# Performance work log

Hardware: AMD Instinct MI355X
Metric: run time of the kernel (lower is better)

## Reference

```python
import jax, jax.numpy as jnp
import numpy as np

BETA = 0.95      # leak
THRESH = 1.0     # snntorch Leaky default threshold
ALPHA = 2.0      # ATan surrogate alpha (atan_with_alpha)
T = 100          # SPIKE_STEPS
D_IN = 65536     # input_dims
HID = 256        # fc1 hidden (hardcoded)
N_OUT = 20       # n_actions(2) * NUM_NEURONS_PER_ACTION(10)


def spike_fn(x):
    # forward of snntorch surrogate.ATan: Heaviside
    return (x > 0.0).astype(x.dtype)


def lif_step(mem, cur):
    # snntorch Leaky, reset_mechanism='subtract':
    # reset computed from previous membrane (detached), then decay+integrate, then fire
    reset = jax.lax.stop_gradient((mem > THRESH).astype(mem.dtype))
    mem_new = BETA * mem + cur - reset * THRESH
    spk = spike_fn(mem_new - THRESH)
    return spk, mem_new


def _run_net(x, W1, b1, W2, b2):
    # x: [T, D_IN]. Precompute all layer-1 currents as one big GEMM, then scan the recurrence.
    cur1_all = x @ W1.T + b1  # [T, HID]

    def step(carry, cur1):
        mem1, mem2 = carry
        spk1, mem1 = lif_step(mem1, cur1)
        cur2 = spk1 @ W2.T + b2  # [n_out]
        spk2, mem2 = lif_step(mem2, cur2)
        return (mem1, mem2), spk2

    init = (jnp.zeros((W1.shape[0],), x.dtype), jnp.zeros((W2.shape[0],), x.dtype))
    (_, mem2_final), spk2_hist = jax.lax.scan(step, init, cur1_all)
    return spk2_hist, mem2_final  # [T, n_out], [n_out]


def setup_inputs() -> dict:
    key = jax.random.key(0)
    ks = jax.random.split(key, 5)
    s = 0.01
    return {
        "poisson_spikes": jax.random.uniform(ks[0], (T, 1, D_IN), dtype=jnp.float32),
        "aW1": jax.random.normal(ks[1], (HID, D_IN), dtype=jnp.float32) * s,
        "ab1": jnp.zeros((HID,), jnp.float32),
        "aW2": jax.random.normal(ks[2], (N_OUT, HID), dtype=jnp.float32) * s,
        "ab2": jnp.zeros((N_OUT,), jnp.float32),
        "cW1": jax.random.normal(ks[3], (HID, D_IN), dtype=jnp.float32) * s,
        "cb1": jnp.zeros((HID,), jnp.float32),
        "cW2": jax.random.normal(ks[4], (1, HID), dtype=jnp.float32) * s,
        "cb2": jnp.zeros((1,), jnp.float32),
    }


def reference(poisson_spikes, aW1, ab1, aW2, ab2, cW1, cb1, cW2, cb2):
    x = poisson_spikes[:, 0, :]  # effective batch of 1 -> [T, D_IN]
    actor_spk_hist, _ = _run_net(x, aW1, ab1, aW2, ab2)        # [T, 20]
    _, critic_mem = _run_net(x, cW1, cb1, cW2, cb2)            # [1]
    spk_sum = actor_spk_hist.sum(axis=0)                       # [20] (sum over timesteps)
    action_vals = jnp.stack([spk_sum[:10].sum(), spk_sum[10:].sum()])
    policy = jax.nn.softmax(action_vals)                       # [2]
    return policy, critic_mem
```

## Files before the change

kernel.cpp:

```cpp
#include <hip/hip_runtime.h>
#include <hip/hip_bf16.h>

#define T_STEPS 100
#define D_IN    65536
#define HID     256
#define HTOT    512
#define BETA    0.95f
#define THRESH  1.0f

typedef __bf16 bf16x8 __attribute__((ext_vector_type(8)));
typedef float  f32x16 __attribute__((ext_vector_type(16)));

__device__ __forceinline__ void gload_lds16(const void* g, void* l) {
    __builtin_amdgcn_global_load_lds(
        (const __attribute__((address_space(1))) void*)g,
        (__attribute__((address_space(3))) void*)l, 16, 0, 0);
}

__global__ __launch_bounds__(512) void k_xpack(
    const float* __restrict__ x, __bf16* __restrict__ xp)
{
    const int idx  = blockIdx.x * 512 + threadIdx.x;
    const int slot = idx & 3;
    const int r    = (idx >> 2) & 127;
    const int gk   = idx >> 9;

    float f[8] = {0.f, 0.f, 0.f, 0.f, 0.f, 0.f, 0.f, 0.f};
    if (r < T_STEPS) {
        const float* src = x + (size_t)r * D_IN + gk * 32 + slot * 8;
        float4 v0 = *(const float4*)src;
        float4 v1 = *(const float4*)(src + 4);
        f[0] = v0.x; f[1] = v0.y; f[2] = v0.z; f[3] = v0.w;
        f[4] = v1.x; f[5] = v1.y; f[6] = v1.z; f[7] = v1.w;
    }
    bf16x8 hi, mi;
#pragma unroll
    for (int e = 0; e < 8; e++) {
        __bf16 h = (__bf16)f[e];
        hi[e] = h; mi[e] = (__bf16)(f[e] - (float)h);
    }
    const int G = r * 4 + (slot ^ ((r >> 1) & 3));
    __bf16* blob = xp + (size_t)gk * 8192;
    *(bf16x8*)(blob + G * 8)        = hi;
    *(bf16x8*)(blob + 4096 + G * 8) = mi;
}

__global__ __launch_bounds__(512, 4) void k_gemm1(
    const float* __restrict__ aW1,
    const float* __restrict__ cW1,
    const __bf16* __restrict__ xp,
    float* __restrict__ P,
    int nsteps)
{
    const int ht   = blockIdx.x;
    const int s    = blockIdx.y;
    const int tid  = threadIdx.x;
    const int lane = tid & 63;
    const int l31  = lane & 31;
    const int wv   = tid >> 6;
    const int wt   = (wv & 1) * 64;
    const int hq   = (wv >> 1) * 32;

    __shared__ __align__(16) char smem[2][32768];

    const float* Wbase = (ht < 2) ? (aW1 + (size_t)ht * 128 * D_IN)
                                  : (cW1 + (size_t)(ht - 2) * 128 * D_IN);

    const int gx0 = wv * 64 + lane;
    const int gx1 = 512 + gx0;
    const int wr0 = gx0 >> 3, wj0 = gx0 & 7;
    const int wr1 = gx1 >> 3, wj1 = gx1 & 7;
    const float* wsrc0 = Wbase + (size_t)wr0 * D_IN + (wj0 ^ (wr0 & 7)) * 4;
    const float* wsrc1 = Wbase + (size_t)wr1 * D_IN + (wj1 ^ (wr1 & 7)) * 4;
    const int gk0 = s * nsteps;

    f32x16 acc0, acc1;
#pragma unroll
    for (int i = 0; i < 16; i++) { acc0[i] = 0.f; acc1[i] = 0.f; }

#define STAGE(i) do {                                                         \
    char* b_ = smem[(i) & 1];                                                 \
    const __bf16* xb_ = xp + (size_t)(gk0 + (i)) * 8192;                      \
    const int kc_ = (gk0 + (i)) * 32;                                         \
    gload_lds16(xb_ + gx0 * 8, b_ + gx0 * 16);                                \
    gload_lds16(xb_ + gx1 * 8, b_ + gx1 * 16);                                \
    gload_lds16(wsrc0 + kc_, b_ + 16384 + gx0 * 16);                          \
    gload_lds16(wsrc1 + kc_, b_ + 16384 + gx1 * 16);                          \
} while (0)

#define COMPUTE(i) do {                                                       \
    const char* b_ = smem[(i) & 1];                                           \
    _Pragma("unroll")                                                         \
    for (int s16 = 0; s16 < 2; s16++) {                                       \
        const int hr = hq + l31;                                              \
        const int gb = s16 * 4 + (lane >> 5) * 2;                             \
        const char* wrow_ = b_ + 16384 + hr * 128;                            \
        float4 wa = *(const float4*)(wrow_ + ((gb ^ (hr & 7)) * 16));         \
        float4 wb = *(const float4*)(wrow_ + (((gb + 1) ^ (hr & 7)) * 16));   \
        float fb[8] = {wa.x, wa.y, wa.z, wa.w, wb.x, wb.y, wb.z, wb.w};       \
        bf16x8 bh, bm;                                                        \
        _Pragma("unroll")                                                     \
        for (int e = 0; e < 8; e++) {                                         \
            __bf16 h = (__bf16)fb[e];                                         \
            bh[e] = h; bm[e] = (__bf16)(fb[e] - (float)h);                    \
        }                                                                     \
        const int slot = s16 * 2 + (lane >> 5);                               \
        const int r0 = wt + l31, r1 = r0 + 32;                                \
        const int G0 = r0 * 4 + (slot ^ ((r0 >> 1) & 3));                     \
        const int G1 = r1 * 4 + (slot ^ ((r1 >> 1) & 3));                     \
        bf16x8 a0h = *(const bf16x8*)(b_ + G0 * 16);                          \
        bf16x8 a0m = *(const bf16x8*)(b_ + 8192 + G0 * 16);                   \
        bf16x8 a1h = *(const bf16x8*)(b_ + G1 * 16);                          \
        bf16x8 a1m = *(const bf16x8*)(b_ + 8192 + G1 * 16);                   \
        acc0 = __builtin_amdgcn_mfma_f32_32x32x16_bf16(a0m, bh, acc0, 0,0,0); \
        acc0 = __builtin_amdgcn_mfma_f32_32x32x16_bf16(a0h, bm, acc0, 0,0,0); \
        acc0 = __builtin_amdgcn_mfma_f32_32x32x16_bf16(a0h, bh, acc0, 0,0,0); \
        acc1 = __builtin_amdgcn_mfma_f32_32x32x16_bf16(a1m, bh, acc1, 0,0,0); \
        acc1 = __builtin_amdgcn_mfma_f32_32x32x16_bf16(a1h, bm, acc1, 0,0,0); \
        acc1 = __builtin_amdgcn_mfma_f32_32x32x16_bf16(a1h, bh, acc1, 0,0,0); \
    }                                                                         \
} while (0)

    STAGE(0);
    STAGE(1);
    for (int i = 0; i < nsteps; i++) {
        if (i + 1 < nsteps) asm volatile("s_waitcnt vmcnt(4)" ::: "memory");
        else                asm volatile("s_waitcnt vmcnt(0)" ::: "memory");
        __builtin_amdgcn_s_barrier();
        __builtin_amdgcn_sched_barrier(0);
        COMPUTE(i);
        __builtin_amdgcn_s_barrier();
        __builtin_amdgcn_sched_barrier(0);
        if (i + 2 < nsteps) STAGE(i + 2);
    }
#undef STAGE
#undef COMPUTE

    const int rbase = 4 * (lane >> 5);
    const int hcol  = ht * 128 + hq + l31;
    float* Pb = P + (size_t)s * T_STEPS * HTOT;
#pragma unroll
    for (int reg = 0; reg < 16; reg++) {
        const int row = (reg & 3) + rbase + 8 * (reg >> 2);
        const int t0  = wt + row;
        const int t1  = wt + 32 + row;
        if (t0 < T_STEPS) Pb[(size_t)t0 * HTOT + hcol] = acc0[reg];
        if (t1 < T_STEPS) Pb[(size_t)t1 * HTOT + hcol] = acc1[reg];
    }
}

__global__ __launch_bounds__(256) void k_reduce(
    const float* __restrict__ P,
    const float* __restrict__ ab1, const float* __restrict__ cb1,
    float* __restrict__ cur1, int NS)
{
    int g4 = blockIdx.x * 256 + threadIdx.x;
    int g  = g4 * 4;
    int h0 = g & (HTOT - 1);
    float4 sum;
    sum.x = (h0 + 0 < HID) ? ab1[h0 + 0] : cb1[h0 + 0 - HID];
    sum.y = (h0 + 1 < HID) ? ab1[h0 + 1] : cb1[h0 + 1 - HID];
    sum.z = (h0 + 2 < HID) ? ab1[h0 + 2] : cb1[h0 + 2 - HID];
    sum.w = (h0 + 3 < HID) ? ab1[h0 + 3] : cb1[h0 + 3 - HID];
    for (int ss = 0; ss < NS; ss++) {
        float4 v = *(const float4*)(P + (size_t)ss * T_STEPS * HTOT + g);
        sum.x += v.x; sum.y += v.y; sum.z += v.z; sum.w += v.w;
    }
    *(float4*)(cur1 + g) = sum;
}

__global__ __launch_bounds__(64) void k_lif1(
    const float* __restrict__ cur1,
    unsigned long long* __restrict__ bitsws,
    float* __restrict__ wsa)
{
    const int b    = blockIdx.x;
    const int lane = threadIdx.x;
    const int n    = b * 64 + lane;

    float mem = 0.f;
    for (int tb = 0; tb < T_STEPS; tb += 10) {
        float c[10];
#pragma unroll
        for (int i = 0; i < 10; i++) c[i] = cur1[(size_t)(tb + i) * HTOT + n];
#pragma unroll
        for (int i = 0; i < 10; i++) {
            float reset = (mem > THRESH) ? THRESH : 0.f;
            mem = BETA * mem + c[i] - reset;
            unsigned long long m = __ballot(mem > THRESH);
            if (lane == 0) bitsws[(size_t)(tb + i) * 8 + b] = m;
        }
    }
    if (b == 0 && lane == 0) { wsa[0] = 0.f; wsa[1] = 0.f; }
}

__global__ __launch_bounds__(128) void k_gemm2(
    const unsigned long long* __restrict__ bitsws,
    const float* __restrict__ aW2, const float* __restrict__ ab2,
    const float* __restrict__ cW2, const float* __restrict__ cb2,
    float* __restrict__ wsa, float* __restrict__ out)
{
    const int j   = blockIdx.x;
    const int tid = threadIdx.x;

    __shared__ float W[256];
    __shared__ float c2[T_STEPS];

    const float* Wsrc = (j < 20) ? (aW2 + j * 256) : cW2;
    for (int i = tid; i < 256; i += 128) W[i] = Wsrc[i];
    const float bias  = (j < 20) ? ab2[j] : cb2[0];
    const int   wbase = (j < 20) ? 0 : 4;
    __syncthreads();

    const int t = tid;
    if (t < T_STEPS) {
        unsigned long long m0 = bitsws[(size_t)t * 8 + wbase + 0];
        unsigned long long m1 = bitsws[(size_t)t * 8 + wbase + 1];
        unsigned long long m2 = bitsws[(size_t)t * 8 + wbase + 2];
        unsigned long long m3 = bitsws[(size_t)t * 8 + wbase + 3];
        float acc = bias;
#pragma unroll
        for (int bitp = 0; bitp < 64; bitp++) {
            acc += ((m0 >> bitp) & 1ULL) ? W[bitp]       : 0.f;
            acc += ((m1 >> bitp) & 1ULL) ? W[64 + bitp]  : 0.f;
            acc += ((m2 >> bitp) & 1ULL) ? W[128 + bitp] : 0.f;
            acc += ((m3 >> bitp) & 1ULL) ? W[192 + bitp] : 0.f;
        }
        c2[t] = acc;
    }
    __syncthreads();

    if (tid == 0) {
        float mem = 0.f, spk = 0.f;
        for (int tt = 0; tt < T_STEPS; tt++) {
            float reset = (mem > THRESH) ? THRESH : 0.f;
            mem = BETA * mem + c2[tt] - reset;
            spk += (mem > THRESH) ? 1.f : 0.f;
        }
        if (j < 10)       atomicAdd(&wsa[0], spk);
        else if (j < 20)  atomicAdd(&wsa[1], spk);
        else              out[2] = mem;
    }
}

__global__ __launch_bounds__(64) void k_final(
    const float* __restrict__ wsa, float* __restrict__ out)
{
    if (threadIdx.x == 0) {
        float a0 = wsa[0], a1 = wsa[1];
        float mx = fmaxf(a0, a1);
        float e0 = expf(a0 - mx), e1 = expf(a1 - mx);
        float inv = 1.f / (e0 + e1);
        out[0] = e0 * inv;
        out[1] = e1 * inv;
    }
}

extern "C" void kernel_launch(void* const* d_in, const int* in_sizes, int n_in,
                              void* d_out, int out_size, void* d_ws, size_t ws_size,
                              hipStream_t stream) {
    const float* x   = (const float*)d_in[0];
    const float* aW1 = (const float*)d_in[1];
    const float* ab1 = (const float*)d_in[2];
    const float* aW2 = (const float*)d_in[3];
    const float* ab2 = (const float*)d_in[4];
    const float* cW1 = (const float*)d_in[5];
    const float* cb1 = (const float*)d_in[6];
    const float* cW2 = (const float*)d_in[7];
    const float* cb2 = (const float*)d_in[8];
    float* out = (float*)d_out;

    const size_t xpack_bytes = 2048ull * 16384;
    int NS = 128;
    while (NS > 8 &&
           xpack_bytes + ((size_t)(NS + 1) * T_STEPS * HTOT) * sizeof(float)
               + 8192 > ws_size)
        NS >>= 1;
    const int nsteps = (D_IN / NS) / 32;

    __bf16* xpack = (__bf16*)d_ws;
    float*  P     = (float*)((char*)d_ws + xpack_bytes);
    float*  cur1  = P + (size_t)NS * T_STEPS * HTOT;
    unsigned long long* bitsws =
        (unsigned long long*)(cur1 + T_STEPS * HTOT);
    float* wsa = (float*)(bitsws + T_STEPS * 8);

    k_xpack <<<2048, 512, 0, stream>>>(x, xpack);
    k_gemm1 <<<dim3(4, NS), 512, 0, stream>>>(aW1, cW1, xpack, P, nsteps);
    k_reduce<<<(T_STEPS * HTOT / 4) / 256, 256, 0, stream>>>(P, ab1, cb1, cur1, NS);
    k_lif1  <<<8, 64, 0, stream>>>(cur1, bitsws, wsa);
    k_gemm2 <<<21, 128, 0, stream>>>(bitsws, aW2, ab2, cW2, cb2, wsa, out);
    k_final <<<1, 64, 0, stream>>>(wsa, out);
}
```

Baseline: 107.7 us.

## Stream x fragments from global in gemm1 and stage only W in LDS

k_gemm1 now uses 256-thread blocks, each covering 64 hidden units, on an 8xNS grid. Only the fp32 W tile goes into double-buffered LDS, now 64 K-columns deep. The packed bf16 hi/lo x fragments are loaded straight from global/L2 inside the compute loop instead of being staged through LDS. k_xpack is remapped so each thread reads contiguous columns of one x row, and it drops its slot swizzle to match the new direct reads. This frees LDS and raises occupancy, at the cost of more global/L2 traffic for x (read by 8 hidden tiles instead of 4) and x-load latency exposed inside the MFMA loop.

```diff
diff --git a/kernel.cpp b/kernel.cpp
--- a/kernel.cpp
+++ b/kernel.cpp
@@ -21,13 +21,13 @@
     const float* __restrict__ x, __bf16* __restrict__ xp)
 {
     const int idx  = blockIdx.x * 512 + threadIdx.x;
-    const int slot = idx & 3;
-    const int r    = (idx >> 2) & 127;
-    const int gk   = idx >> 9;
+    const int r    = idx >> 13;
+    const int cidx = idx & 8191;
+    const int col  = cidx * 8;
 
     float f[8] = {0.f, 0.f, 0.f, 0.f, 0.f, 0.f, 0.f, 0.f};
     if (r < T_STEPS) {
-        const float* src = x + (size_t)r * D_IN + gk * 32 + slot * 8;
+        const float* src = x + (size_t)r * D_IN + col;
         float4 v0 = *(const float4*)src;
         float4 v1 = *(const float4*)(src + 4);
         f[0] = v0.x; f[1] = v0.y; f[2] = v0.z; f[3] = v0.w;
@@ -39,13 +39,15 @@
         __bf16 h = (__bf16)f[e];
         hi[e] = h; mi[e] = (__bf16)(f[e] - (float)h);
     }
-    const int G = r * 4 + (slot ^ ((r >> 1) & 3));
+    const int gk   = col >> 5;
+    const int slot = (col >> 3) & 3;
+    const int G    = r * 4 + slot;
     __bf16* blob = xp + (size_t)gk * 8192;
     *(bf16x8*)(blob + G * 8)        = hi;
     *(bf16x8*)(blob + 4096 + G * 8) = mi;
 }
 
-__global__ __launch_bounds__(512, 4) void k_gemm1(
+__global__ __launch_bounds__(256, 4) void k_gemm1(
     const float* __restrict__ aW1,
     const float* __restrict__ cW1,
     const __bf16* __restrict__ xp,
@@ -57,46 +59,60 @@
     const int tid  = threadIdx.x;
     const int lane = tid & 63;
     const int l31  = lane & 31;
+    const int h5   = lane >> 5;
     const int wv   = tid >> 6;
     const int wt   = (wv & 1) * 64;
-    const int hq   = (wv >> 1) * 32;
-
-    __shared__ __align__(16) char smem[2][32768];
-
-    const float* Wbase = (ht < 2) ? (aW1 + (size_t)ht * 128 * D_IN)
-                                  : (cW1 + (size_t)(ht - 2) * 128 * D_IN);
-
-    const int gx0 = wv * 64 + lane;
-    const int gx1 = 512 + gx0;
-    const int wr0 = gx0 >> 3, wj0 = gx0 & 7;
-    const int wr1 = gx1 >> 3, wj1 = gx1 & 7;
-    const float* wsrc0 = Wbase + (size_t)wr0 * D_IN + (wj0 ^ (wr0 & 7)) * 4;
-    const float* wsrc1 = Wbase + (size_t)wr1 * D_IN + (wj1 ^ (wr1 & 7)) * 4;
-    const int gk0 = s * nsteps;
+    const int wh   = (wv >> 1) * 32;
+
+    __shared__ __align__(16) char Wlds[2][16384];
+
+    const float* Wbase = (ht < 4) ? (aW1 + (size_t)ht * 64 * D_IN)
+                                  : (cW1 + (size_t)(ht - 4) * 64 * D_IN);
+
+    int   wgrow[4];
+    const float* wgsrc[4];
+#pragma unroll
+    for (int o = 0; o < 4; o++) {
+        const int idx = o * 256 + tid;
+        const int row = idx >> 4, g = idx & 15;
+        wgrow[o] = idx;
+        wgsrc[o] = Wbase + (size_t)row * D_IN + (g ^ (row & 7)) * 4;
+    }
+    const int kb0 = s * (nsteps * 64);
+    const int gk0 = s * (nsteps * 2);
 
     f32x16 acc0, acc1;
 #pragma unroll
     for (int i = 0; i < 16; i++) { acc0[i] = 0.f; acc1[i] = 0.f; }
 
 #define STAGE(i) do {                                                         \
-    char* b_ = smem[(i) & 1];                                                 \
-    const __bf16* xb_ = xp + (size_t)(gk0 + (i)) * 8192;                      \
-    const int kc_ = (gk0 + (i)) * 32;                                         \
-    gload_lds16(xb_ + gx0 * 8, b_ + gx0 * 16);                                \
-    gload_lds16(xb_ + gx1 * 8, b_ + gx1 * 16);                                \
-    gload_lds16(wsrc0 + kc_, b_ + 16384 + gx0 * 16);                          \
-    gload_lds16(wsrc1 + kc_, b_ + 16384 + gx1 * 16);                          \
+    char* b_ = Wlds[(i) & 1];                                                 \
+    const int kb_ = kb0 + (i) * 64;                                           \
+    _Pragma("unroll")                                                         \
+    for (int o = 0; o < 4; o++)                                               \
+        gload_lds16(wgsrc[o] + kb_, b_ + wgrow[o] * 16);                      \
 } while (0)
 
 #define COMPUTE(i) do {                                                       \
-    const char* b_ = smem[(i) & 1];                                           \
+    const char* b_ = Wlds[(i) & 1];                                           \
     _Pragma("unroll")                                                         \
-    for (int s16 = 0; s16 < 2; s16++) {                                       \
-        const int hr = hq + l31;                                              \
-        const int gb = s16 * 4 + (lane >> 5) * 2;                             \
-        const char* wrow_ = b_ + 16384 + hr * 128;                            \
-        float4 wa = *(const float4*)(wrow_ + ((gb ^ (hr & 7)) * 16));         \
-        float4 wb = *(const float4*)(wrow_ + (((gb + 1) ^ (hr & 7)) * 16));   \
+    for (int s16 = 0; s16 < 4; s16++) {                                       \
+           \
+        const __bf16* blob_ = xp + (size_t)(gk0 + (i) * 2 + (s16 >> 1)) * 8192;\
+        const int slot_ = (s16 & 1) * 2 + h5;                                 \
+        const int r0_ = wt + l31, r1_ = r0_ + 32;                             \
+        const __bf16* pa0_ = blob_ + (r0_ * 4 + slot_) * 8;                   \
+        const __bf16* pa1_ = blob_ + (r1_ * 4 + slot_) * 8;                   \
+        bf16x8 a0h = *(const bf16x8*)(pa0_);                                  \
+        bf16x8 a0m = *(const bf16x8*)(pa0_ + 4096);                          \
+        bf16x8 a1h = *(const bf16x8*)(pa1_);                                  \
+        bf16x8 a1m = *(const bf16x8*)(pa1_ + 4096);                          \
+                              \
+        const int hr_ = wh + l31;                                             \
+        const int c0_ = (s16 * 4 + h5 * 2)     ^ (hr_ & 7);                   \
+        const int c1_ = (s16 * 4 + h5 * 2 + 1) ^ (hr_ & 7);                   \
+        float4 wa = *(const float4*)(b_ + (hr_ * 16 + c0_) * 16);             \
+        float4 wb = *(const float4*)(b_ + (hr_ * 16 + c1_) * 16);             \
         float fb[8] = {wa.x, wa.y, wa.z, wa.w, wb.x, wb.y, wb.z, wb.w};       \
         bf16x8 bh, bm;                                                        \
         _Pragma("unroll")                                                     \
@@ -104,14 +120,6 @@
             __bf16 h = (__bf16)fb[e];                                         \
             bh[e] = h; bm[e] = (__bf16)(fb[e] - (float)h);                    \
         }                                                                     \
-        const int slot = s16 * 2 + (lane >> 5);                               \
-        const int r0 = wt + l31, r1 = r0 + 32;                                \
-        const int G0 = r0 * 4 + (slot ^ ((r0 >> 1) & 3));                     \
-        const int G1 = r1 * 4 + (slot ^ ((r1 >> 1) & 3));                     \
-        bf16x8 a0h = *(const bf16x8*)(b_ + G0 * 16);                          \
-        bf16x8 a0m = *(const bf16x8*)(b_ + 8192 + G0 * 16);                   \
-        bf16x8 a1h = *(const bf16x8*)(b_ + G1 * 16);                          \
-        bf16x8 a1m = *(const bf16x8*)(b_ + 8192 + G1 * 16);                   \
         acc0 = __builtin_amdgcn_mfma_f32_32x32x16_bf16(a0m, bh, acc0, 0,0,0); \
         acc0 = __builtin_amdgcn_mfma_f32_32x32x16_bf16(a0h, bm, acc0, 0,0,0); \
         acc0 = __builtin_amdgcn_mfma_f32_32x32x16_bf16(a0h, bh, acc0, 0,0,0); \
@@ -136,8 +144,8 @@
 #undef STAGE
 #undef COMPUTE
 
-    const int rbase = 4 * (lane >> 5);
-    const int hcol  = ht * 128 + hq + l31;
+    const int rbase = 4 * h5;
+    const int hcol  = ht * 64 + wh + l31;
     float* Pb = P + (size_t)s * T_STEPS * HTOT;
 #pragma unroll
     for (int reg = 0; reg < 16; reg++) {
@@ -276,7 +284,7 @@
            xpack_bytes + ((size_t)(NS + 1) * T_STEPS * HTOT) * sizeof(float)
                + 8192 > ws_size)
         NS >>= 1;
-    const int nsteps = (D_IN / NS) / 32;
+    const int nsteps = (D_IN / NS) / 64;
 
     __bf16* xpack = (__bf16*)d_ws;
     float*  P     = (float*)((char*)d_ws + xpack_bytes);
@@ -286,7 +294,7 @@
     float* wsa = (float*)(bitsws + T_STEPS * 8);
 
     k_xpack <<<2048, 512, 0, stream>>>(x, xpack);
-    k_gemm1 <<<dim3(4, NS), 512, 0, stream>>>(aW1, cW1, xpack, P, nsteps);
+    k_gemm1 <<<dim3(8, NS), 256, 0, stream>>>(aW1, cW1, xpack, P, nsteps);
     k_reduce<<<(T_STEPS * HTOT / 4) / 256, 256, 0, stream>>>(P, ab1, cb1, cur1, NS);
     k_lif1  <<<8, 64, 0, stream>>>(cur1, bitsws, wsa);
     k_gemm2 <<<21, 128, 0, stream>>>(bitsws, aW2, ab2, cW2, cb2, wsa, out);
```

Measured after the change: 124.3 us. +15.4%, slower.

## Retile layer-1 GEMM to 32-column blocks and fuse split-K reduce into LIF

Applied to the files above, without the earlier changes.

The layer-1 GEMM now uses 256-thread blocks, each covering 32 hidden columns across all 128 time rows, so there are 16 column tiles instead of 4 and a smaller LDS footprint per block. The split-K count drops from 128 to 64. The separate reduce kernel is merged into the LIF kernel, which sums the partials into shared memory before running the recurrence, removing one launch and the cur1 round trip. In exchange, the x tile is re-read by four times as many column blocks, and the fused reduce runs on only 8 blocks, which may be slow.

```diff
diff --git a/kernel.cpp b/kernel.cpp
--- a/kernel.cpp
+++ b/kernel.cpp
@@ -45,7 +45,7 @@
     *(bf16x8*)(blob + 4096 + G * 8) = mi;
 }
 
-__global__ __launch_bounds__(512, 4) void k_gemm1(
+__global__ __launch_bounds__(256, 4) void k_gemm1(
     const float* __restrict__ aW1,
     const float* __restrict__ cW1,
     const __bf16* __restrict__ xp,
@@ -57,46 +57,44 @@
     const int tid  = threadIdx.x;
     const int lane = tid & 63;
     const int l31  = lane & 31;
+    const int h5   = lane >> 5;
     const int wv   = tid >> 6;
-    const int wt   = (wv & 1) * 64;
-    const int hq   = (wv >> 1) * 32;
-
-    __shared__ __align__(16) char smem[2][32768];
-
-    const float* Wbase = (ht < 2) ? (aW1 + (size_t)ht * 128 * D_IN)
-                                  : (cW1 + (size_t)(ht - 2) * 128 * D_IN);
-
-    const int gx0 = wv * 64 + lane;
-    const int gx1 = 512 + gx0;
-    const int wr0 = gx0 >> 3, wj0 = gx0 & 7;
-    const int wr1 = gx1 >> 3, wj1 = gx1 & 7;
-    const float* wsrc0 = Wbase + (size_t)wr0 * D_IN + (wj0 ^ (wr0 & 7)) * 4;
-    const float* wsrc1 = Wbase + (size_t)wr1 * D_IN + (wj1 ^ (wr1 & 7)) * 4;
+    const int wt   = wv * 32;
+
+    __shared__ __align__(16) char smem[2][20480];
+
+    const float* Wbase = (ht < 8) ? (aW1 + (size_t)ht * 32 * D_IN)
+                                  : (cW1 + (size_t)(ht - 8) * 32 * D_IN);
+
+    const int wrow = tid >> 3, wg = tid & 7;
+    const float* wsrc = Wbase + (size_t)wrow * D_IN + (wg ^ (wrow & 7)) * 4;
     const int gk0 = s * nsteps;
 
-    f32x16 acc0, acc1;
-#pragma unroll
-    for (int i = 0; i < 16; i++) { acc0[i] = 0.f; acc1[i] = 0.f; }
+    f32x16 acc;
+#pragma unroll
+    for (int i = 0; i < 16; i++) acc[i] = 0.f;
 
 #define STAGE(i) do {                                                         \
     char* b_ = smem[(i) & 1];                                                 \
     const __bf16* xb_ = xp + (size_t)(gk0 + (i)) * 8192;                      \
     const int kc_ = (gk0 + (i)) * 32;                                         \
-    gload_lds16(xb_ + gx0 * 8, b_ + gx0 * 16);                                \
-    gload_lds16(xb_ + gx1 * 8, b_ + gx1 * 16);                                \
-    gload_lds16(wsrc0 + kc_, b_ + 16384 + gx0 * 16);                          \
-    gload_lds16(wsrc1 + kc_, b_ + 16384 + gx1 * 16);                          \
+    gload_lds16(xb_ + (tid +   0) * 8, b_ + (tid +   0) * 16);                \
+    gload_lds16(xb_ + (tid + 256) * 8, b_ + (tid + 256) * 16);                \
+    gload_lds16(xb_ + (tid + 512) * 8, b_ + (tid + 512) * 16);                \
+    gload_lds16(xb_ + (tid + 768) * 8, b_ + (tid + 768) * 16);                \
+    gload_lds16(wsrc + kc_, b_ + 16384 + tid * 16);                           \
 } while (0)
 
 #define COMPUTE(i) do {                                                       \
     const char* b_ = smem[(i) & 1];                                           \
     _Pragma("unroll")                                                         \
     for (int s16 = 0; s16 < 2; s16++) {                                       \
-        const int hr = hq + l31;                                              \
-        const int gb = s16 * 4 + (lane >> 5) * 2;                             \
-        const char* wrow_ = b_ + 16384 + hr * 128;                            \
-        float4 wa = *(const float4*)(wrow_ + ((gb ^ (hr & 7)) * 16));         \
-        float4 wb = *(const float4*)(wrow_ + (((gb + 1) ^ (hr & 7)) * 16));   \
+                              \
+        const int hr_ = l31;                                                  \
+        const int gb_ = s16 * 4 + h5 * 2;                                     \
+        const char* wrow_ = b_ + 16384 + hr_ * 128;                           \
+        float4 wa = *(const float4*)(wrow_ + ((gb_ ^ (hr_ & 7)) * 16));       \
+        float4 wb = *(const float4*)(wrow_ + (((gb_ + 1) ^ (hr_ & 7)) * 16)); \
         float fb[8] = {wa.x, wa.y, wa.z, wa.w, wb.x, wb.y, wb.z, wb.w};       \
         bf16x8 bh, bm;                                                        \
         _Pragma("unroll")                                                     \
@@ -104,27 +102,22 @@
             __bf16 h = (__bf16)fb[e];                                         \
             bh[e] = h; bm[e] = (__bf16)(fb[e] - (float)h);                    \
         }                                                                     \
-        const int slot = s16 * 2 + (lane >> 5);                               \
-        const int r0 = wt + l31, r1 = r0 + 32;                                \
-        const int G0 = r0 * 4 + (slot ^ ((r0 >> 1) & 3));                     \
-        const int G1 = r1 * 4 + (slot ^ ((r1 >> 1) & 3));                     \
-        bf16x8 a0h = *(const bf16x8*)(b_ + G0 * 16);                          \
-        bf16x8 a0m = *(const bf16x8*)(b_ + 8192 + G0 * 16);                   \
-        bf16x8 a1h = *(const bf16x8*)(b_ + G1 * 16);                          \
-        bf16x8 a1m = *(const bf16x8*)(b_ + 8192 + G1 * 16);                   \
-        acc0 = __builtin_amdgcn_mfma_f32_32x32x16_bf16(a0m, bh, acc0, 0,0,0); \
-        acc0 = __builtin_amdgcn_mfma_f32_32x32x16_bf16(a0h, bm, acc0, 0,0,0); \
-        acc0 = __builtin_amdgcn_mfma_f32_32x32x16_bf16(a0h, bh, acc0, 0,0,0); \
-        acc1 = __builtin_amdgcn_mfma_f32_32x32x16_bf16(a1m, bh, acc1, 0,0,0); \
-        acc1 = __builtin_amdgcn_mfma_f32_32x32x16_bf16(a1h, bm, acc1, 0,0,0); \
-        acc1 = __builtin_amdgcn_mfma_f32_32x32x16_bf16(a1h, bh, acc1, 0,0,0); \
+                                         \
+        const int slot_ = s16 * 2 + h5;                                       \
+        const int r0_   = wt + l31;                                           \
+        const int G0_   = r0_ * 4 + (slot_ ^ ((r0_ >> 1) & 3));               \
+        bf16x8 a0h = *(const bf16x8*)(b_ + G0_ * 16);                         \
+        bf16x8 a0m = *(const bf16x8*)(b_ + 8192 + G0_ * 16);                  \
+        acc = __builtin_amdgcn_mfma_f32_32x32x16_bf16(a0m, bh, acc, 0, 0, 0); \
+        acc = __builtin_amdgcn_mfma_f32_32x32x16_bf16(a0h, bm, acc, 0, 0, 0); \
+        acc = __builtin_amdgcn_mfma_f32_32x32x16_bf16(a0h, bh, acc, 0, 0, 0); \
     }                                                                         \
 } while (0)
 
     STAGE(0);
     STAGE(1);
     for (int i = 0; i < nsteps; i++) {
-        if (i + 1 < nsteps) asm volatile("s_waitcnt vmcnt(4)" ::: "memory");
+        if (i + 1 < nsteps) asm volatile("s_waitcnt vmcnt(5)" ::: "memory");
         else                asm volatile("s_waitcnt vmcnt(0)" ::: "memory");
         __builtin_amdgcn_s_barrier();
         __builtin_amdgcn_sched_barrier(0);
@@ -136,62 +129,47 @@
 #undef STAGE
 #undef COMPUTE
 
-    const int rbase = 4 * (lane >> 5);
-    const int hcol  = ht * 128 + hq + l31;
+    const int hcol = ht * 32 + l31;
     float* Pb = P + (size_t)s * T_STEPS * HTOT;
 #pragma unroll
     for (int reg = 0; reg < 16; reg++) {
-        const int row = (reg & 3) + rbase + 8 * (reg >> 2);
-        const int t0  = wt + row;
-        const int t1  = wt + 32 + row;
-        if (t0 < T_STEPS) Pb[(size_t)t0 * HTOT + hcol] = acc0[reg];
-        if (t1 < T_STEPS) Pb[(size_t)t1 * HTOT + hcol] = acc1[reg];
-    }
-}
-
-__global__ __launch_bounds__(256) void k_reduce(
+        const int t = wt + (reg & 3) + 4 * h5 + 8 * (reg >> 2);
+        if (t < T_STEPS) Pb[(size_t)t * HTOT + hcol] = acc[reg];
+    }
+}
+
+__global__ __launch_bounds__(512) void k_rlif(
     const float* __restrict__ P,
     const float* __restrict__ ab1, const float* __restrict__ cb1,
-    float* __restrict__ cur1, int NS)
-{
-    int g4 = blockIdx.x * 256 + threadIdx.x;
-    int g  = g4 * 4;
-    int h0 = g & (HTOT - 1);
-    float4 sum;
-    sum.x = (h0 + 0 < HID) ? ab1[h0 + 0] : cb1[h0 + 0 - HID];
-    sum.y = (h0 + 1 < HID) ? ab1[h0 + 1] : cb1[h0 + 1 - HID];
-    sum.z = (h0 + 2 < HID) ? ab1[h0 + 2] : cb1[h0 + 2 - HID];
-    sum.w = (h0 + 3 < HID) ? ab1[h0 + 3] : cb1[h0 + 3 - HID];
-    for (int ss = 0; ss < NS; ss++) {
-        float4 v = *(const float4*)(P + (size_t)ss * T_STEPS * HTOT + g);
-        sum.x += v.x; sum.y += v.y; sum.z += v.z; sum.w += v.w;
-    }
-    *(float4*)(cur1 + g) = sum;
-}
-
-__global__ __launch_bounds__(64) void k_lif1(
-    const float* __restrict__ cur1,
     unsigned long long* __restrict__ bitsws,
-    float* __restrict__ wsa)
-{
-    const int b    = blockIdx.x;
-    const int lane = threadIdx.x;
-    const int n    = b * 64 + lane;
-
-    float mem = 0.f;
-    for (int tb = 0; tb < T_STEPS; tb += 10) {
-        float c[10];
-#pragma unroll
-        for (int i = 0; i < 10; i++) c[i] = cur1[(size_t)(tb + i) * HTOT + n];
-#pragma unroll
-        for (int i = 0; i < 10; i++) {
+    float* __restrict__ wsa, int NS)
+{
+    const int b   = blockIdx.x;
+    const int n0  = b * 64;
+    const int tid = threadIdx.x;
+
+    __shared__ float cur1L[T_STEPS][64];
+
+    for (int idx = tid; idx < T_STEPS * 64; idx += 512) {
+        const int c = idx & 63, t = idx >> 6;
+        const int h = n0 + c;
+        float sum = (h < HID) ? ab1[h] : cb1[h - HID];
+        for (int ss = 0; ss < NS; ss++)
+            sum += P[(size_t)ss * T_STEPS * HTOT + (size_t)t * HTOT + h];
+        cur1L[t][c] = sum;
+    }
+    __syncthreads();
+
+    if (tid < 64) {
+        float mem = 0.f;
+        for (int t = 0; t < T_STEPS; t++) {
             float reset = (mem > THRESH) ? THRESH : 0.f;
-            mem = BETA * mem + c[i] - reset;
+            mem = BETA * mem + cur1L[t][tid] - reset;
             unsigned long long m = __ballot(mem > THRESH);
-            if (lane == 0) bitsws[(size_t)(tb + i) * 8 + b] = m;
+            if (tid == 0) bitsws[(size_t)t * 8 + b] = m;
         }
     }
-    if (b == 0 && lane == 0) { wsa[0] = 0.f; wsa[1] = 0.f; }
+    if (b == 0 && tid == 0) { wsa[0] = 0.f; wsa[1] = 0.f; }
 }
 
 __global__ __launch_bounds__(128) void k_gemm2(
@@ -271,24 +249,22 @@
     float* out = (float*)d_out;
 
     const size_t xpack_bytes = 2048ull * 16384;
-    int NS = 128;
+    int NS = 64;
     while (NS > 8 &&
-           xpack_bytes + ((size_t)(NS + 1) * T_STEPS * HTOT) * sizeof(float)
+           xpack_bytes + ((size_t)NS * T_STEPS * HTOT) * sizeof(float)
                + 8192 > ws_size)
         NS >>= 1;
     const int nsteps = (D_IN / NS) / 32;
 
     __bf16* xpack = (__bf16*)d_ws;
     float*  P     = (float*)((char*)d_ws + xpack_bytes);
-    float*  cur1  = P + (size_t)NS * T_STEPS * HTOT;
     unsigned long long* bitsws =
-        (unsigned long long*)(cur1 + T_STEPS * HTOT);
+        (unsigned long long*)(P + (size_t)NS * T_STEPS * HTOT);
     float* wsa = (float*)(bitsws + T_STEPS * 8);
 
     k_xpack <<<2048, 512, 0, stream>>>(x, xpack);
-    k_gemm1 <<<dim3(4, NS), 512, 0, stream>>>(aW1, cW1, xpack, P, nsteps);
-    k_reduce<<<(T_STEPS * HTOT / 4) / 256, 256, 0, stream>>>(P, ab1, cb1, cur1, NS);
-    k_lif1  <<<8, 64, 0, stream>>>(cur1, bitsws, wsa);
+    k_gemm1 <<<dim3(16, NS), 256, 0, stream>>>(aW1, cW1, xpack, P, nsteps);
+    k_rlif  <<<8, 512, 0, stream>>>(P, ab1, cb1, bitsws, wsa, NS);
     k_gemm2 <<<21, 128, 0, stream>>>(bitsws, aW2, ab2, cW2, cb2, wsa, out);
     k_final <<<1, 64, 0, stream>>>(wsa, out);
 }
```

After: 293.8 us. +172.7%, slower.
